# Optimization experiments

Measured on AMD Instinct MI355X. Metric: run time of the kernel, lower is better.

Reference implementation:

```python
import jax, jax.numpy as jnp
import numpy as np

HEAD_DIM = 32
KS = 3            # kernel_size
DIL = 2           # dilation
PAD = DIL * (KS - 1) // 2
SCALE = HEAD_DIM ** (-0.5)


def _unfold(x):
    """nn.ReflectionPad2d(PAD) + nn.Unfold(KS, dilation=DIL).
    x: [B, C, H, W] -> [B, C, KS*KS, H, W] with kernel positions row-major,
    matching nn.Unfold's (C, kh, kw) channel ordering."""
    B, C, H, W = x.shape
    xp = jnp.pad(x, ((0, 0), (0, 0), (PAD, PAD), (PAD, PAD)), mode='reflect')
    patches = jnp.stack(
        [xp[:, :, i * DIL:i * DIL + H, j * DIL:j * DIL + W]
         for i in range(KS) for j in range(KS)],
        axis=2,
    )
    return patches  # [B, C, ksq, H, W]


def setup_inputs() -> dict:
    key = jax.random.key(0)
    kq, kk, kv = jax.random.split(key, 3)
    shape = (16, 384, 56, 56)
    return {
        'q': jax.random.normal(kq, shape, dtype=jnp.float32),
        'k': jax.random.normal(kk, shape, dtype=jnp.float32),
        'v': jax.random.normal(kv, shape, dtype=jnp.float32),
    }


def reference(q, k, v):
    B, d, H, W = q.shape
    nH = d // HEAD_DIM
    ksq = KS * KS
    # q: [B, nH, headDim, H, W]
    q_r = q.reshape(B, nH, HEAD_DIM, H, W)
    # k/v unfolded: [B, nH, headDim, ksq, H, W]
    k_p = _unfold(k).reshape(B, nH, HEAD_DIM, ksq, H, W)
    v_p = _unfold(v).reshape(B, nH, HEAD_DIM, ksq, H, W)
    # attention scores over the ksq local window
    attn = jnp.einsum('bnchw,bnckhw->bnkhw', q_r, k_p) * SCALE
    attn = jax.nn.softmax(attn, axis=2)
    out = jnp.einsum('bnkhw,bnckhw->bnchw', attn, v_p)
    # [B, nH, headDim, H, W] -> [B, H, W, nH*headDim]
    out = out.reshape(B, d, H, W).transpose(0, 2, 3, 1)
    return out
```

## Files before the change

### kernel.cpp

```cpp
#include <hip/hip_runtime.h>
#include <stdint.h>


#define BB 16
#define CH 384
#define HH 56
#define WW 56
#define NH 12
#define DD 32
#define HW (HH * WW)
#define KSQ 9
#define SCALE 0.17677669529663687f

#define BAND 8
#define DCH 8
#define NCHUNK (DD / DCH)
#define MAXROWS 12
#define SLICE (MAXROWS * WW)
#define LBUF (DCH * SLICE)

__device__ __forceinline__ void async16(const void* g, void* l) {
    __builtin_amdgcn_global_load_lds(
        (const __attribute__((address_space(1))) void*)g,
        (__attribute__((address_space(3))) void*)l, 16, 0, 0);
}

__device__ __forceinline__ void stage_chunk(const float* __restrict__ plane0,
                                            float* ldsbuf, int Sbytes,
                                            int wv, int lane) {
    const int lo16 = lane * 16;
    for (int s = wv; s < DCH; s += 7) {
        const char* g = (const char*)(plane0 + s * HW);
        char* l = (char*)(ldsbuf + s * SLICE);
        async16(g + lo16, l + lo16);
        async16(g + 1024 + lo16, l + 1024 + lo16);
        const int t = Sbytes - 1024;
        async16(g + t + lo16, l + t + lo16);
    }
}

__global__ __launch_bounds__(448, 5)
void dilate_attn_kernel(const float* __restrict__ q,
                        const float* __restrict__ k,
                        const float* __restrict__ v,
                        float* __restrict__ out) {
    __shared__ float lds[2][LBUF];

    const int band = blockIdx.x;
    const int n    = blockIdx.y;
    const int b    = blockIdx.z;

    const int tid  = threadIdx.x;
    const int lane = tid & 63;
    const int wv   = tid >> 6;

    const int w = tid % WW;
    const int r = tid / WW;
    const int h0 = band * BAND;
    const int h  = h0 + r;

    const int lo = (h0 - 2 < 0) ? 0 : h0 - 2;
    const int hi = (h0 + 9 > HH - 1) ? HH - 1 : h0 + 9;
    const int Sbytes = (hi - lo + 1) * WW * 4;

    int off9[KSQ];
    {
        int wc[3];
#pragma unroll
        for (int j = 0; j < 3; ++j) {
            int c = w + 2 * (j - 1);
            c = (c < 0) ? -c : ((c >= WW) ? (2 * WW - 2 - c) : c);
            wc[j] = c;
        }
#pragma unroll
        for (int i = 0; i < 3; ++i) {
            int rr = h + 2 * (i - 1);
            rr = (rr < 0) ? -rr : ((rr >= HH) ? (2 * HH - 2 - rr) : rr);
            rr -= lo;
#pragma unroll
            for (int j = 0; j < 3; ++j) off9[i * 3 + j] = rr * WW + wc[j];
        }
    }

    const int planebase = (b * CH + n * DD) * HW;
    const float* qp = q + planebase + h * WW + w;
    const float* kstage = k + planebase + lo * WW;
    const float* vstage = v + planebase + lo * WW;

    float sc[KSQ];
#pragma unroll
    for (int ii = 0; ii < KSQ; ++ii) sc[ii] = 0.f;

    stage_chunk(kstage, lds[0], Sbytes, wv, lane);
    __syncthreads();
    int cur = 0;

    for (int c = 0; c < NCHUNK; ++c) {
        if (c < NCHUNK - 1)
            stage_chunk(kstage + (c + 1) * DCH * HW, lds[cur ^ 1], Sbytes, wv, lane);
        else
            stage_chunk(vstage, lds[cur ^ 1], Sbytes, wv, lane);

        float qd[DCH];
#pragma unroll
        for (int j = 0; j < DCH; ++j) qd[j] = qp[(c * DCH + j) * HW];

        const float* Bf = lds[cur];
#pragma unroll
        for (int j = 0; j < DCH; ++j) {
            const float* Ls = Bf + j * SLICE;
            const float qj = qd[j];
#pragma unroll
            for (int ii = 0; ii < KSQ; ++ii)
                sc[ii] = fmaf(qj, Ls[off9[ii]], sc[ii]);
        }
        __syncthreads();
        cur ^= 1;
    }

    {
        float m = sc[0];
#pragma unroll
        for (int ii = 1; ii < KSQ; ++ii) m = fmaxf(m, sc[ii]);
        float sum = 0.f;
#pragma unroll
        for (int ii = 0; ii < KSQ; ++ii) {
            sc[ii] = __expf((sc[ii] - m) * SCALE);
            sum += sc[ii];
        }
        const float inv = 1.f / sum;
#pragma unroll
        for (int ii = 0; ii < KSQ; ++ii) sc[ii] *= inv;
    }

    float* op = out + ((b * HH + h) * WW + w) * CH + n * DD;

    for (int c = 0; c < NCHUNK; ++c) {
        if (c < NCHUNK - 1)
            stage_chunk(vstage + (c + 1) * DCH * HW, lds[cur ^ 1], Sbytes, wv, lane);

        const float* Bf = lds[cur];
        float o[DCH];
#pragma unroll
        for (int j = 0; j < DCH; ++j) {
            const float* Ls = Bf + j * SLICE;
            float acc = 0.f;
#pragma unroll
            for (int ii = 0; ii < KSQ; ++ii)
                acc = fmaf(sc[ii], Ls[off9[ii]], acc);
            o[j] = acc;
        }
        *(float4*)(op + c * DCH)     = make_float4(o[0], o[1], o[2], o[3]);
        *(float4*)(op + c * DCH + 4) = make_float4(o[4], o[5], o[6], o[7]);

        if (c < NCHUNK - 1) {
            __syncthreads();
            cur ^= 1;
        }
    }
}

extern "C" void kernel_launch(void* const* d_in, const int* in_sizes, int n_in,
                              void* d_out, int out_size, void* d_ws, size_t ws_size,
                              hipStream_t stream) {
    const float* q = (const float*)d_in[0];
    const float* k = (const float*)d_in[1];
    const float* v = (const float*)d_in[2];
    float* out = (float*)d_out;

    dim3 grid(HH / BAND, NH, BB);
    dilate_attn_kernel<<<grid, 448, 0, stream>>>(q, k, v, out);
}
```

Baseline: 279.5 us.

## Use shared-base window loads with selects, preload q, and defer output stores

Replaces the nine per-thread LDS offsets with one base address per kernel row plus constant offsets 0/2/4. Reflection at the left and right edges is handled by selects between the loaded values. This lets LDS reads use immediate offsets and cuts the address registers. It also preloads all 32 q values before the first sync, holds all 32 outputs in registers so they are written in one burst at the end, fully unrolls the chunk loops, and lowers launch bounds occupancy from 5 to 4. The higher register use may reduce occupancy. The LDS buffer gets 4 floats of padding so the shifted reads near w=55 stay in range.

```diff
diff --git a/kernel.cpp b/kernel.cpp
--- a/kernel.cpp
+++ b/kernel.cpp
@@ -1,5 +1,4 @@
 #include <hip/hip_runtime.h>
-#include <stdint.h>
 
 
 #define BB 16
@@ -39,12 +38,20 @@
     }
 }
 
-__global__ __launch_bounds__(448, 5)
+#define WIN3(p, v0, v1, v2)                          \
+    do {                                             \
+        float A_ = (p)[0], B_ = (p)[2], C_ = (p)[4]; \
+        v0 = isW0 ? B_ : A_;                         \
+        v1 = wle1 ? A_ : B_;                         \
+        v2 = isW55 ? A_ : (midB ? B_ : C_);          \
+    } while (0)
+
+__global__ __launch_bounds__(448, 4)
 void dilate_attn_kernel(const float* __restrict__ q,
                         const float* __restrict__ k,
                         const float* __restrict__ v,
                         float* __restrict__ out) {
-    __shared__ float lds[2][LBUF];
+    __shared__ float lds[2][LBUF + 4];
 
     const int band = blockIdx.x;
     const int n    = blockIdx.y;
@@ -63,23 +70,18 @@
     const int hi = (h0 + 9 > HH - 1) ? HH - 1 : h0 + 9;
     const int Sbytes = (hi - lo + 1) * WW * 4;
 
-    int off9[KSQ];
-    {
-        int wc[3];
+    const int cb    = (w < 2) ? w : (w - 2);
+    const bool isW0  = (w == 0);
+    const bool wle1  = (w <= 1);
+    const bool midB  = (w < 2) || (w == 54);
+    const bool isW55 = (w == 55);
+
+    int rb[3];
 #pragma unroll
-        for (int j = 0; j < 3; ++j) {
-            int c = w + 2 * (j - 1);
-            c = (c < 0) ? -c : ((c >= WW) ? (2 * WW - 2 - c) : c);
-            wc[j] = c;
-        }
-#pragma unroll
-        for (int i = 0; i < 3; ++i) {
-            int rr = h + 2 * (i - 1);
-            rr = (rr < 0) ? -rr : ((rr >= HH) ? (2 * HH - 2 - rr) : rr);
-            rr -= lo;
-#pragma unroll
-            for (int j = 0; j < 3; ++j) off9[i * 3 + j] = rr * WW + wc[j];
-        }
+    for (int i = 0; i < 3; ++i) {
+        int rr = h + 2 * (i - 1);
+        rr = (rr < 0) ? -rr : ((rr >= HH) ? (2 * HH - 2 - rr) : rr);
+        rb[i] = (rr - lo) * WW + cb;
     }
 
     const int planebase = (b * CH + n * DD) * HW;
@@ -87,32 +89,40 @@
     const float* kstage = k + planebase + lo * WW;
     const float* vstage = v + planebase + lo * WW;
 
+    stage_chunk(kstage, lds[0], Sbytes, wv, lane);
+
+    float qreg[DD];
+#pragma unroll
+    for (int d = 0; d < DD; ++d) qreg[d] = qp[d * HW];
+
     float sc[KSQ];
 #pragma unroll
     for (int ii = 0; ii < KSQ; ++ii) sc[ii] = 0.f;
 
-    stage_chunk(kstage, lds[0], Sbytes, wv, lane);
     __syncthreads();
     int cur = 0;
 
+#pragma unroll
     for (int c = 0; c < NCHUNK; ++c) {
         if (c < NCHUNK - 1)
             stage_chunk(kstage + (c + 1) * DCH * HW, lds[cur ^ 1], Sbytes, wv, lane);
         else
             stage_chunk(vstage, lds[cur ^ 1], Sbytes, wv, lane);
 
-        float qd[DCH];
-#pragma unroll
-        for (int j = 0; j < DCH; ++j) qd[j] = qp[(c * DCH + j) * HW];
-
         const float* Bf = lds[cur];
 #pragma unroll
         for (int j = 0; j < DCH; ++j) {
             const float* Ls = Bf + j * SLICE;
-            const float qj = qd[j];
+            const float qj = qreg[c * DCH + j];
 #pragma unroll
-            for (int ii = 0; ii < KSQ; ++ii)
-                sc[ii] = fmaf(qj, Ls[off9[ii]], sc[ii]);
+            for (int i = 0; i < 3; ++i) {
+                const float* p = Ls + rb[i];
+                float v0, v1, v2;
+                WIN3(p, v0, v1, v2);
+                sc[i * 3 + 0] = fmaf(qj, v0, sc[i * 3 + 0]);
+                sc[i * 3 + 1] = fmaf(qj, v1, sc[i * 3 + 1]);
+                sc[i * 3 + 2] = fmaf(qj, v2, sc[i * 3 + 2]);
+            }
         }
         __syncthreads();
         cur ^= 1;
@@ -133,30 +143,43 @@
         for (int ii = 0; ii < KSQ; ++ii) sc[ii] *= inv;
     }
 
-    float* op = out + ((b * HH + h) * WW + w) * CH + n * DD;
+    float o[DD];
+#pragma unroll
+    for (int d = 0; d < DD; ++d) o[d] = 0.f;
 
+#pragma unroll
     for (int c = 0; c < NCHUNK; ++c) {
         if (c < NCHUNK - 1)
             stage_chunk(vstage + (c + 1) * DCH * HW, lds[cur ^ 1], Sbytes, wv, lane);
 
         const float* Bf = lds[cur];
-        float o[DCH];
 #pragma unroll
         for (int j = 0; j < DCH; ++j) {
             const float* Ls = Bf + j * SLICE;
             float acc = 0.f;
 #pragma unroll
-            for (int ii = 0; ii < KSQ; ++ii)
-                acc = fmaf(sc[ii], Ls[off9[ii]], acc);
-            o[j] = acc;
+            for (int i = 0; i < 3; ++i) {
+                const float* p = Ls + rb[i];
+                float v0, v1, v2;
+                WIN3(p, v0, v1, v2);
+                acc = fmaf(sc[i * 3 + 0], v0,
+                      fmaf(sc[i * 3 + 1], v1,
+                      fmaf(sc[i * 3 + 2], v2, acc)));
+            }
+            o[c * DCH + j] = acc;
         }
-        *(float4*)(op + c * DCH)     = make_float4(o[0], o[1], o[2], o[3]);
-        *(float4*)(op + c * DCH + 4) = make_float4(o[4], o[5], o[6], o[7]);
-
         if (c < NCHUNK - 1) {
             __syncthreads();
             cur ^= 1;
         }
+    }
+
+    float* op = out + ((b * HH + h) * WW + w) * CH + n * DD;
+#pragma unroll
+    for (int d4 = 0; d4 < DD / 4; ++d4) {
+        *(float4*)(op + d4 * 4) =
+            make_float4(o[d4 * 4 + 0], o[d4 * 4 + 1],
+                        o[d4 * 4 + 2], o[d4 * 4 + 3]);
     }
 }
 
```

Result: slower. 1.098 ms (+292.9%).
